# Performance work log

Hardware: AMD Instinct MI355X
Metric: run time of the kernel (lower is better)

## Reference

```python
import math
import jax, jax.numpy as jnp
import numpy as np

N_HEAD = 16
ROPE_BASE = 10000.0


def _rope_tables(T, half, dtype):
    # build_sin_cos(seq_len, dim=head_dim//2): inv freq of length `half`
    pos = jnp.arange(T, dtype=jnp.float32)[:, None]                       # (T,1)
    inv = jnp.exp(jnp.arange(0, 2 * half, 2, dtype=jnp.float32) * (-math.log(ROPE_BASE) / (2 * half)))
    ang = pos * inv                                                        # (T, half)
    return jnp.sin(ang).astype(dtype), jnp.cos(ang).astype(dtype)


def _apply_rope(q, k, sin, cos):
    # q,k: (B,T,H,Dh); sin,cos: (T, Dh//2) -> broadcast over batch and heads
    half = q.shape[-1] // 2
    s = sin[None, :, None, :]
    c = cos[None, :, None, :]
    q1, q2 = q[..., :half], q[..., half:]
    k1, k2 = k[..., :half], k[..., half:]
    q = jnp.concatenate([q1 * c - q2 * s, q2 * c + q1 * s], axis=-1)
    k = jnp.concatenate([k1 * c - k2 * s, k2 * c + k1 * s], axis=-1)
    return q, k


def setup_inputs() -> dict:
    key = jax.random.key(0)
    k1, k2, k3 = jax.random.split(key, 3)
    B, T, C = 2, 2048, 2048
    x = jax.random.normal(k1, (B, T, C), dtype=jnp.float32)
    w_qkv = jax.random.normal(k2, (3 * C, C), dtype=jnp.float32) * (1.0 / math.sqrt(C))
    w_proj = jax.random.normal(k3, (C, C), dtype=jnp.float32) * (1.0 / math.sqrt(C))
    return {"x": x, "w_qkv": w_qkv, "w_proj": w_proj}


def reference(x, w_qkv, w_proj):
    B, T, C = x.shape
    H = N_HEAD
    Dh = C // H
    # fused QKV projection (Linear, no bias): (B,T,3C) -> (B,T,3,H,Dh)
    qkv = jnp.einsum('btc,oc->bto', x, w_qkv).reshape(B, T, 3, H, Dh)
    q, k, v = qkv[:, :, 0], qkv[:, :, 1], qkv[:, :, 2]          # (B,T,H,Dh)
    sin, cos = _rope_tables(T, Dh // 2, x.dtype)
    q, k = _apply_rope(q, k, sin, cos)
    # causal attention, scale 1/sqrt(Dh) (flash default softmax_scale=None)
    scale = 1.0 / math.sqrt(Dh)
    scores = jnp.einsum('bqhd,bkhd->bhqk', q, k) * scale        # (B,H,T,T)
    mask = jnp.tril(jnp.ones((T, T), dtype=bool))
    scores = jnp.where(mask[None, None], scores, jnp.finfo(scores.dtype).min)
    probs = jax.nn.softmax(scores, axis=-1)
    out = jnp.einsum('bhqk,bkhd->bqhd', probs, v)               # (B,T,H,Dh)
    # faithful to original: permute(0,2,1,3) then reshape_as(x)
    out = jnp.transpose(out, (0, 2, 1, 3)).reshape(B, T, C)
    return jnp.einsum('btc,oc->bto', out, w_proj)
```

## Files before the change

kernel.cpp:

```cpp
#include <hip/hip_runtime.h>
#include <hip/hip_bf16.h>

typedef __bf16 bf16_t;
typedef __bf16 bf16x8 __attribute__((ext_vector_type(8)));
typedef float f32x4 __attribute__((ext_vector_type(4)));

#define MFMA16(a, b, c) __builtin_amdgcn_mfma_f32_16x16x32_bf16(a, b, c, 0, 0, 0)

__device__ __forceinline__ void async_copy16(const void* g, void* l) {
  __builtin_amdgcn_global_load_lds(
      (const __attribute__((address_space(1))) void*)g,
      (__attribute__((address_space(3))) void*)l, 16, 0, 0);
}

__global__ void cast_f32_bf16(const float* __restrict__ in, bf16_t* __restrict__ out, int n8) {
  int stride = gridDim.x * blockDim.x;
  for (int i = blockIdx.x * blockDim.x + threadIdx.x; i < n8; i += stride) {
    const float* p = in + (size_t)i * 8;
    f32x4 a = *(const f32x4*)p;
    f32x4 b = *(const f32x4*)(p + 4);
    bf16x8 o;
    o[0] = (bf16_t)a[0]; o[1] = (bf16_t)a[1]; o[2] = (bf16_t)a[2]; o[3] = (bf16_t)a[3];
    o[4] = (bf16_t)b[0]; o[5] = (bf16_t)b[1]; o[6] = (bf16_t)b[2]; o[7] = (bf16_t)b[3];
    *(bf16x8*)(out + (size_t)i * 8) = o;
  }
}

template <int MODE>
__global__ __launch_bounds__(512, 2) void gemm256(
    const bf16_t* __restrict__ A, const bf16_t* __restrict__ Bw, float* __restrict__ C,
    bf16_t* __restrict__ qo, bf16_t* __restrict__ ko, bf16_t* __restrict__ vto,
    int M, int N, int K, int nby) {
  __shared__ __align__(16) char lds[147456];
  int tid = threadIdx.x;
  int w = tid >> 6, lane = tid & 63;
  int wm = w >> 1, wn = w & 1;
  int mr = lane & 15, kg = lane >> 4;

  int nwg = gridDim.x;
  int orig = blockIdx.x;
  int wgid = (orig & 7) * (nwg >> 3) + (orig >> 3);
  int by = wgid % nby, bx = wgid / nby;
  int row0 = by * 256, col0 = bx * 128;

  size_t aoff[4], boff[2];
#pragma unroll
  for (int it = 0; it < 4; ++it) {
    int c = tid + it * 512;
    int r = c >> 3;
    int chs = (c & 7) ^ (r & 7);
    aoff[it] = (size_t)(row0 + r) * K + chs * 8;
  }
#pragma unroll
  for (int it = 0; it < 2; ++it) {
    int c = tid + it * 512;
    int r = c >> 3;
    int chs = (c & 7) ^ (r & 7);
    boff[it] = (size_t)(col0 + r) * K + chs * 8;
  }

  auto stageA = [&](int buf, int kt, int half) {
    char* Ad = &lds[buf * 49152];
#pragma unroll
    for (int it = half * 2; it < half * 2 + 2; ++it)
      async_copy16(A + aoff[it] + kt * 64, Ad + (tid + it * 512) * 16);
  };
  auto stageB = [&](int buf, int kt) {
    char* Bd = &lds[buf * 49152 + 32768];
#pragma unroll
    for (int it = 0; it < 2; ++it)
      async_copy16(Bw + boff[it] + kt * 64, Bd + (tid + it * 512) * 16);
  };

  f32x4 zero = {0.f, 0.f, 0.f, 0.f};
  f32x4 acc[4][4];
#pragma unroll
  for (int mi = 0; mi < 4; ++mi)
#pragma unroll
    for (int ni = 0; ni < 4; ++ni) acc[mi][ni] = zero;

  int nt = K >> 6;
  stageA(0, 0, 0); stageA(0, 0, 1); stageB(0, 0);
  stageA(1, 1, 0); stageA(1, 1, 1); stageB(1, 1);
  asm volatile("s_waitcnt vmcnt(6)" ::: "memory");
  __builtin_amdgcn_sched_barrier(0);
  __builtin_amdgcn_s_barrier();
  __builtin_amdgcn_sched_barrier(0);

#pragma unroll 1
  for (int t = 0; t < nt; ++t) {
    int cur = t % 3;
    int nxt = (t + 2) % 3;
    int kt2 = (t + 2 < nt) ? (t + 2) : t;
    const char* Ab = &lds[cur * 49152];
    const char* Bb = &lds[cur * 49152 + 32768];
    bf16x8 af[4][2], bfr[4][2];
#pragma unroll
    for (int mi = 0; mi < 4; ++mi) {
      int row = wm * 64 + mi * 16 + mr;
      const char* rb = Ab + row * 128;
      int sz = (row & 7) << 4;
      af[mi][0] = *(const bf16x8*)(rb + ((kg * 16) ^ sz));
      af[mi][1] = *(const bf16x8*)(rb + ((64 + kg * 16) ^ sz));
    }
#pragma unroll
    for (int ni = 0; ni < 4; ++ni) {
      int row = wn * 64 + ni * 16 + mr;
      const char* rb = Bb + row * 128;
      int sz = (row & 7) << 4;
      bfr[ni][0] = *(const bf16x8*)(rb + ((kg * 16) ^ sz));
      bfr[ni][1] = *(const bf16x8*)(rb + ((64 + kg * 16) ^ sz));
    }
    stageA(nxt, kt2, 0);
    __builtin_amdgcn_s_setprio(1);
#pragma unroll
    for (int mi = 0; mi < 4; ++mi) {
      acc[mi][0] = MFMA16(af[mi][0], bfr[0][0], acc[mi][0]);
      acc[mi][0] = MFMA16(af[mi][1], bfr[0][1], acc[mi][0]);
    }
    __builtin_amdgcn_s_setprio(0);
    stageA(nxt, kt2, 1);
    __builtin_amdgcn_s_setprio(1);
#pragma unroll
    for (int mi = 0; mi < 4; ++mi) {
      acc[mi][1] = MFMA16(af[mi][0], bfr[1][0], acc[mi][1]);
      acc[mi][1] = MFMA16(af[mi][1], bfr[1][1], acc[mi][1]);
    }
    __builtin_amdgcn_s_setprio(0);
    stageB(nxt, kt2);
    __builtin_amdgcn_s_setprio(1);
#pragma unroll
    for (int mi = 0; mi < 4; ++mi) {
      acc[mi][2] = MFMA16(af[mi][0], bfr[2][0], acc[mi][2]);
      acc[mi][2] = MFMA16(af[mi][1], bfr[2][1], acc[mi][2]);
      acc[mi][3] = MFMA16(af[mi][0], bfr[3][0], acc[mi][3]);
      acc[mi][3] = MFMA16(af[mi][1], bfr[3][1], acc[mi][3]);
    }
    __builtin_amdgcn_s_setprio(0);
    asm volatile("s_waitcnt vmcnt(6)" ::: "memory");
    __builtin_amdgcn_sched_barrier(0);
    __builtin_amdgcn_s_barrier();
    __builtin_amdgcn_sched_barrier(0);
  }
  asm volatile("s_waitcnt vmcnt(0)" ::: "memory");
  __syncthreads();

  if (MODE == 0) {
#pragma unroll
    for (int mi = 0; mi < 4; ++mi)
#pragma unroll
      for (int ni = 0; ni < 4; ++ni)
#pragma unroll
        for (int jj = 0; jj < 4; ++jj) {
          int row = row0 + wm * 64 + mi * 16 + kg * 4 + jj;
          int col = col0 + wn * 64 + ni * 16 + mr;
          C[(size_t)row * N + col] = acc[mi][ni][jj];
        }
  } else {
    char* tb = &lds[0];
    int s = col0 >> 11, h = (col0 >> 7) & 15;
    int b = row0 >> 11, t0 = row0 & 2047;
    if (s < 2) {
#pragma unroll
      for (int mi = 0; mi < 4; ++mi)
#pragma unroll
        for (int ni = 0; ni < 4; ++ni)
#pragma unroll
          for (int jj = 0; jj < 4; ++jj) {
            int rloc = wm * 64 + mi * 16 + kg * 4 + jj;
            int cb = (wn * 64 + ni * 16 + mr) * 2;
            *(bf16_t*)(tb + rloc * 256 + (cb ^ ((rloc & 7) << 4))) = (bf16_t)acc[mi][ni][jj];
          }
      __syncthreads();
      int r = tid >> 1, hh = tid & 1;
      const char* rowb = tb + r * 256;
      int sz = (r & 7) << 4;
      int t = t0 + r;
      bf16_t* dst = (s == 0 ? qo : ko) + ((size_t)((b * 16 + h) * 2048 + t)) * 128 + hh * 64;
      float tf = (float)t;
      const float cinv = -0.20762050593046014f;
#pragma unroll
      for (int m = 0; m < 8; ++m) {
        bf16x8 va = *(const bf16x8*)(rowb + ((hh * 128 + m * 16) ^ sz));
        bf16x8 vb = *(const bf16x8*)(rowb + (((hh ^ 1) * 128 + m * 16) ^ sz));
        bf16x8 o;
#pragma unroll
        for (int e = 0; e < 8; ++e) {
          float ang = tf * exp2f((float)(m * 8 + e) * cinv);
          float sv = __sinf(ang), cv = __cosf(ang);
          float x1 = (float)va[e], x2 = (float)vb[e];
          o[e] = (bf16_t)((hh == 0) ? (x1 * cv - x2 * sv) : (x1 * cv + x2 * sv));
        }
        *(bf16x8*)(dst + m * 8) = o;
      }
    } else {
#pragma unroll
      for (int mi = 0; mi < 4; ++mi)
#pragma unroll
        for (int ni = 0; ni < 4; ++ni)
#pragma unroll
          for (int jj = 0; jj < 4; ++jj) {
            int rloc = wm * 64 + mi * 16 + kg * 4 + jj;
            int cloc = wn * 64 + ni * 16 + mr;
            *(bf16_t*)(tb + cloc * 512 + ((rloc * 2) ^ ((cloc & 7) << 4))) =
                (bf16_t)acc[mi][ni][jj];
          }
      __syncthreads();
      int d = tid >> 2, qt = tid & 3;
      const char* rowb = tb + d * 512;
      int sz = (d & 7) << 4;
      bf16_t* dst = vto + ((size_t)((b * 16 + h) * 128 + d)) * 2048 + t0 + qt * 64;
#pragma unroll
      for (int m2 = 0; m2 < 8; ++m2)
        *(bf16x8*)(dst + m2 * 8) = *(const bf16x8*)(rowb + ((qt * 128 + m2 * 16) ^ sz));
    }
  }
}

__global__ __launch_bounds__(256) void attn_kernel(
    const bf16_t* __restrict__ qg, const bf16_t* __restrict__ kgl,
    const bf16_t* __restrict__ vtg, bf16_t* __restrict__ og) {
  __shared__ __align__(16) bf16_t Ks[2][64 * 128];
  __shared__ __align__(16) bf16_t Vs[2][128 * 64];
  __shared__ __align__(16) bf16_t plds[4][1024];
  const int T = 2048;
  int tid = threadIdx.x;
  int w = tid >> 6, lane = tid & 63;
  int mr = lane & 15, kg = lane >> 4;
  int swz = (mr & 7) << 4;

  int L = blockIdx.y * 16 + blockIdx.x;
  int role = (L & 7) * 64 + (L >> 3);
  int bx = role & 15, bh = role >> 4;

  const bf16_t* Q = qg + (size_t)bh * T * 128;
  const bf16_t* K = kgl + (size_t)bh * T * 128;
  const bf16_t* Vt = vtg + (size_t)bh * 128 * T;

  int sb = tid * 16;
  int krl = sb >> 8;
  int kc = (sb & 255) ^ ((krl & 7) << 4);
  size_t ksrc = (size_t)krl * 128 + (kc >> 1);
  int vdl = sb >> 7;
  int vc = (sb & 127) ^ ((vdl & 7) << 4);
  size_t vsrc = (size_t)vdl * 2048 + (vc >> 1);

  auto stage = [&](int buf, int kb) {
#pragma unroll
    for (int it = 0; it < 4; ++it)
      async_copy16(K + (size_t)(kb + it * 16) * 128 + ksrc, &Ks[buf][it * 2048 + tid * 8]);
#pragma unroll
    for (int it = 0; it < 4; ++it)
      async_copy16(Vt + (size_t)it * 65536 + kb + vsrc, &Vs[buf][it * 2048 + tid * 8]);
  };

  const float cscale = 0.12751744f;
  f32x4 zero = {0.f, 0.f, 0.f, 0.f};
  bf16_t* P = &plds[w][0];
  int b = bh >> 4, h = bh & 15;

#pragma unroll 1
  for (int ph = 0; ph < 2; ++ph) {
    int qb = ph ? bx : (31 - bx);
    int qr0 = qb * 64 + w * 16;
    bf16x8 qf[4];
#pragma unroll
    for (int db = 0; db < 4; ++db)
      qf[db] = *(const bf16x8*)(Q + (size_t)(qr0 + mr) * 128 + db * 32 + kg * 8);

    f32x4 acc[8];
#pragma unroll
    for (int d2 = 0; d2 < 8; ++d2) acc[d2] = zero;
    float mrun[4] = {-1e30f, -1e30f, -1e30f, -1e30f};
    float lrun[4] = {0.f, 0.f, 0.f, 0.f};

    int nj = qb + 1;
    __syncthreads();
    stage(0, 0);
    int cur = 0;
#pragma unroll 1
    for (int j = 0; j < nj; ++j) {
      __syncthreads();
      if (j + 1 < nj) stage(cur ^ 1, (j + 1) * 64);
      const char* KsB = (const char*)&Ks[cur][0];
      const char* VsB = (const char*)&Vs[cur][0];
      int kb = j * 64;
      f32x4 s[4];
#pragma unroll
      for (int ntl = 0; ntl < 4; ++ntl) {
        s[ntl] = zero;
        int rowb = (ntl * 16 + mr) * 256;
#pragma unroll
        for (int db = 0; db < 4; ++db) {
          bf16x8 kf = *(const bf16x8*)(KsB + rowb + ((db * 64 + kg * 16) ^ swz));
          s[ntl] = MFMA16(qf[db], kf, s[ntl]);
        }
      }
      float pvv[4][4];
      float tmax[4] = {-3e38f, -3e38f, -3e38f, -3e38f};
      bool diag = (j == qb);
#pragma unroll
      for (int ntl = 0; ntl < 4; ++ntl)
#pragma unroll
        for (int jj = 0; jj < 4; ++jj) {
          float v = s[ntl][jj] * cscale;
          if (diag && (kb + ntl * 16 + mr) > (qr0 + kg * 4 + jj)) v = -1e30f;
          pvv[ntl][jj] = v;
          tmax[jj] = fmaxf(tmax[jj], v);
        }
#pragma unroll
      for (int m = 1; m < 16; m <<= 1)
#pragma unroll
        for (int jj = 0; jj < 4; ++jj)
          tmax[jj] = fmaxf(tmax[jj], __shfl_xor(tmax[jj], m, 64));
      bool ok = true;
#pragma unroll
      for (int jj = 0; jj < 4; ++jj) ok &= (tmax[jj] <= mrun[jj] + 8.0f);
      if (!__all(ok)) {
#pragma unroll
        for (int jj = 0; jj < 4; ++jj) {
          float mn = fmaxf(mrun[jj], tmax[jj]);
          float corr = __builtin_amdgcn_exp2f(mrun[jj] - mn);
          mrun[jj] = mn;
          lrun[jj] *= corr;
#pragma unroll
          for (int d2 = 0; d2 < 8; ++d2) acc[d2][jj] *= corr;
        }
      }
      float rs[4] = {0.f, 0.f, 0.f, 0.f};
#pragma unroll
      for (int ntl = 0; ntl < 4; ++ntl)
#pragma unroll
        for (int jj = 0; jj < 4; ++jj) {
          float p = __builtin_amdgcn_exp2f(pvv[ntl][jj] - mrun[jj]);
          pvv[ntl][jj] = p;
          rs[jj] += p;
        }
#pragma unroll
      for (int m = 1; m < 16; m <<= 1)
#pragma unroll
        for (int jj = 0; jj < 4; ++jj) rs[jj] += __shfl_xor(rs[jj], m, 64);
#pragma unroll
      for (int jj = 0; jj < 4; ++jj) lrun[jj] += rs[jj];
#pragma unroll
      for (int ntl = 0; ntl < 4; ++ntl)
#pragma unroll
        for (int jj = 0; jj < 4; ++jj) {
          int rr = kg * 4 + jj;
          int cbyte = (mr + ntl * 16) * 2;
          *(bf16_t*)((char*)P + rr * 128 + (cbyte ^ ((rr & 7) << 4))) = (bf16_t)pvv[ntl][jj];
        }
#pragma unroll
      for (int ks = 0; ks < 2; ++ks) {
        int cb = (ks * 32 + kg * 8) * 2;
        bf16x8 pa = *(const bf16x8*)((const char*)P + mr * 128 + (cb ^ ((mr & 7) << 4)));
#pragma unroll
        for (int d2 = 0; d2 < 8; ++d2) {
          bf16x8 vf = *(const bf16x8*)(VsB + (d2 * 16 + mr) * 128 + ((ks * 64 + kg * 16) ^ swz));
          acc[d2] = MFMA16(pa, vf, acc[d2]);
        }
      }
      cur ^= 1;
    }
#pragma unroll
    for (int jj = 0; jj < 4; ++jj) {
      float invl = 1.0f / lrun[jj];
      int t = qr0 + kg * 4 + jj;
      size_t row = (size_t)b * 2048 + h * 128 + (t >> 4);
      bf16_t* orow = og + row * 2048 + (t & 15) * 128;
#pragma unroll
      for (int d2 = 0; d2 < 8; ++d2)
        orow[d2 * 16 + mr] = (bf16_t)(acc[d2][jj] * invl);
    }
  }
}

extern "C" void kernel_launch(void* const* d_in, const int* in_sizes, int n_in,
                              void* d_out, int out_size, void* d_ws, size_t ws_size,
                              hipStream_t stream) {
  const float* x = (const float*)d_in[0];
  const float* wqkv = (const float*)d_in[1];
  const float* wproj = (const float*)d_in[2];
  float* out = (float*)d_out;
  char* ws = (char*)d_ws;

  const size_t OFF_WQKV = 16777216;
  const size_t OFF_Q = 41943040;
  const size_t OFF_K = 58720256;
  const size_t OFF_VT = 75497472;

  bf16_t* xb = (bf16_t*)(ws);
  bf16_t* wqkvb = (bf16_t*)(ws + OFF_WQKV);
  bf16_t* g_q = (bf16_t*)(ws + OFF_Q);
  bf16_t* g_k = (bf16_t*)(ws + OFF_K);
  bf16_t* g_vt = (bf16_t*)(ws + OFF_VT);
  bf16_t* g_att = (bf16_t*)(ws);
  bf16_t* wprojb = (bf16_t*)(ws + OFF_WQKV);

  cast_f32_bf16<<<2048, 256, 0, stream>>>(x, xb, 8388608 / 8);
  cast_f32_bf16<<<2048, 256, 0, stream>>>(wqkv, wqkvb, 12582912 / 8);
  gemm256<1><<<768, 512, 0, stream>>>(xb, wqkvb, nullptr, g_q, g_k, g_vt,
                                      4096, 6144, 2048, 16);
  cast_f32_bf16<<<2048, 256, 0, stream>>>(wproj, wprojb, 4194304 / 8);
  attn_kernel<<<dim3(16, 32), 256, 0, stream>>>(g_q, g_k, g_vt, g_att);
  gemm256<0><<<256, 512, 0, stream>>>(g_att, wprojb, out, nullptr, nullptr, nullptr,
                                      4096, 2048, 2048, 16);
}
```

Before: 277.7 us.

## Add dedicated 256x256-tile QKV GEMM with 4-stage pipeline and fused RoPE epilogue

Replaces the templated 256x128-tile GEMM used for the QKV projection with a dedicated kernel that uses 256x256 output tiles, a 32-wide K step and a four-buffer async LDS pipeline, launched on 384 blocks instead of 768. Each block now covers two heads, so the RoPE epilogue writes both rotated halves per thread and the V-transpose epilogue covers two heads. The larger tile raises arithmetic intensity and halves the global reads per output. The cost is more accumulator registers per thread (128 floats) and fewer blocks to fill the CUs. The output-projection GEMM is trimmed to its plain fp32 store path.

```diff
diff --git a/kernel.cpp b/kernel.cpp
--- a/kernel.cpp
+++ b/kernel.cpp
@@ -26,10 +26,168 @@
   }
 }
 
+__global__ __launch_bounds__(512, 2) void gemm_qkv(
+    const bf16_t* __restrict__ A, const bf16_t* __restrict__ Bw,
+    bf16_t* __restrict__ qo, bf16_t* __restrict__ ko, bf16_t* __restrict__ vto,
+    int K) {
+  __shared__ __align__(16) char lds[131072];
+  int tid = threadIdx.x;
+  int w = tid >> 6, lane = tid & 63;
+  int wm = w & 1, wn = w >> 1;
+  int mr = lane & 15, kg = lane >> 4;
+
+  int orig = blockIdx.x;
+  int chunk = orig & 7, i = orig >> 3;
+  int by = (chunk & 3) * 4 + (i & 3);
+  int bx = (chunk >> 2) * 12 + (i >> 2);
+  int row0 = by * 256, col0 = bx * 256;
+
+  size_t aoff[2], boff[2];
+#pragma unroll
+  for (int it = 0; it < 2; ++it) {
+    int c = tid + it * 512;
+    int r = c >> 2;
+    int lc = (c & 3) ^ ((r >> 1) & 3);
+    aoff[it] = (size_t)(row0 + r) * K + lc * 8;
+    boff[it] = (size_t)(col0 + r) * K + lc * 8;
+  }
+
+  auto stageA = [&](int buf, int kt) {
+    char* Ad = &lds[buf * 32768];
+#pragma unroll
+    for (int it = 0; it < 2; ++it)
+      async_copy16(A + aoff[it] + kt * 32, Ad + (tid + it * 512) * 16);
+  };
+  auto stageB = [&](int buf, int kt) {
+    char* Bd = &lds[buf * 32768 + 16384];
+#pragma unroll
+    for (int it = 0; it < 2; ++it)
+      async_copy16(Bw + boff[it] + kt * 32, Bd + (tid + it * 512) * 16);
+  };
+
+  f32x4 zero = {0.f, 0.f, 0.f, 0.f};
+  f32x4 acc[8][4];
+#pragma unroll
+  for (int mi = 0; mi < 8; ++mi)
+#pragma unroll
+    for (int ni = 0; ni < 4; ++ni) acc[mi][ni] = zero;
+
+  int nt = K >> 5;
+  stageA(0, 0); stageB(0, 0);
+  stageA(1, 1); stageB(1, 1);
+  stageA(2, 2); stageB(2, 2);
+  asm volatile("s_waitcnt vmcnt(8)" ::: "memory");
+  __builtin_amdgcn_sched_barrier(0);
+  __builtin_amdgcn_s_barrier();
+  __builtin_amdgcn_sched_barrier(0);
+
+#pragma unroll 1
+  for (int t = 0; t < nt; ++t) {
+    int cur = t & 3;
+    int nb = (t + 3) & 3;
+    int kt3 = (t + 3 < nt) ? (t + 3) : (nt - 1);
+    const char* Ab = &lds[cur * 32768];
+    const char* Bb = &lds[cur * 32768 + 16384];
+    bf16x8 af[8], bfr[4];
+#pragma unroll
+    for (int mi = 0; mi < 8; ++mi) {
+      int r = wm * 128 + mi * 16 + mr;
+      af[mi] = *(const bf16x8*)(Ab + r * 64 + ((kg ^ ((r >> 1) & 3)) << 4));
+    }
+#pragma unroll
+    for (int ni = 0; ni < 4; ++ni) {
+      int r = wn * 64 + ni * 16 + mr;
+      bfr[ni] = *(const bf16x8*)(Bb + r * 64 + ((kg ^ ((r >> 1) & 3)) << 4));
+    }
+    stageA(nb, kt3);
+    __builtin_amdgcn_s_setprio(1);
+#pragma unroll
+    for (int mi = 0; mi < 8; ++mi) acc[mi][0] = MFMA16(af[mi], bfr[0], acc[mi][0]);
+#pragma unroll
+    for (int mi = 0; mi < 8; ++mi) acc[mi][1] = MFMA16(af[mi], bfr[1], acc[mi][1]);
+    __builtin_amdgcn_s_setprio(0);
+    stageB(nb, kt3);
+    __builtin_amdgcn_s_setprio(1);
+#pragma unroll
+    for (int mi = 0; mi < 8; ++mi) acc[mi][2] = MFMA16(af[mi], bfr[2], acc[mi][2]);
+#pragma unroll
+    for (int mi = 0; mi < 8; ++mi) acc[mi][3] = MFMA16(af[mi], bfr[3], acc[mi][3]);
+    __builtin_amdgcn_s_setprio(0);
+    asm volatile("s_waitcnt vmcnt(8)" ::: "memory");
+    __builtin_amdgcn_sched_barrier(0);
+    __builtin_amdgcn_s_barrier();
+    __builtin_amdgcn_sched_barrier(0);
+  }
+  asm volatile("s_waitcnt vmcnt(0)" ::: "memory");
+  __syncthreads();
+
+  char* tb = &lds[0];
+  int s = col0 >> 11;
+  int h0 = (col0 >> 7) & 15;
+  int b = row0 >> 11, t0 = row0 & 2047;
+  if (s < 2) {
+#pragma unroll
+    for (int mi = 0; mi < 8; ++mi)
+#pragma unroll
+      for (int ni = 0; ni < 4; ++ni)
+#pragma unroll
+        for (int jj = 0; jj < 4; ++jj) {
+          int rl = wm * 128 + mi * 16 + kg * 4 + jj;
+          int cb = (wn * 64 + ni * 16 + mr) * 2;
+          *(bf16_t*)(tb + rl * 512 + (cb ^ ((rl & 7) << 4))) = (bf16_t)acc[mi][ni][jj];
+        }
+    __syncthreads();
+    int r = tid >> 1, hs = tid & 1;
+    const char* rowb = tb + r * 512;
+    int sz = (r & 7) << 4;
+    int t = t0 + r;
+    bf16_t* dst = (s == 0 ? qo : ko) + ((size_t)((b * 16 + h0 + hs) * 2048 + t)) * 128;
+    float tf = (float)t;
+    const float cinv = -0.20762050593046014f;
+    bf16x8 vin[16];
+#pragma unroll
+    for (int m = 0; m < 16; ++m)
+      vin[m] = *(const bf16x8*)(rowb + ((hs * 256 + m * 16) ^ sz));
+#pragma unroll
+    for (int m = 0; m < 8; ++m) {
+      bf16x8 o1, o2;
+#pragma unroll
+      for (int e = 0; e < 8; ++e) {
+        float ang = tf * exp2f((float)(m * 8 + e) * cinv);
+        float sv = __sinf(ang), cv = __cosf(ang);
+        float x1 = (float)vin[m][e], x2 = (float)vin[m + 8][e];
+        o1[e] = (bf16_t)(x1 * cv - x2 * sv);
+        o2[e] = (bf16_t)(x2 * cv + x1 * sv);
+      }
+      *(bf16x8*)(dst + m * 8) = o1;
+      *(bf16x8*)(dst + 64 + m * 8) = o2;
+    }
+  } else {
+#pragma unroll
+    for (int mi = 0; mi < 8; ++mi)
+#pragma unroll
+      for (int ni = 0; ni < 4; ++ni)
+#pragma unroll
+        for (int jj = 0; jj < 4; ++jj) {
+          int rl = wm * 128 + mi * 16 + kg * 4 + jj;
+          int cl = wn * 64 + ni * 16 + mr;
+          *(bf16_t*)(tb + cl * 512 + ((rl * 2) ^ ((cl & 7) << 4))) = (bf16_t)acc[mi][ni][jj];
+        }
+    __syncthreads();
+    int d = tid >> 1, ts = tid & 1;
+    const char* rowb = tb + d * 512;
+    int sz = (d & 7) << 4;
+    bf16_t* dst = vto + ((size_t)((b * 16 + h0 + (d >> 7)) * 128 + (d & 127))) * 2048 +
+                  t0 + ts * 128;
+#pragma unroll
+    for (int m = 0; m < 16; ++m)
+      *(bf16x8*)(dst + m * 8) = *(const bf16x8*)(rowb + ((ts * 256 + m * 16) ^ sz));
+  }
+}
+
 template <int MODE>
 __global__ __launch_bounds__(512, 2) void gemm256(
     const bf16_t* __restrict__ A, const bf16_t* __restrict__ Bw, float* __restrict__ C,
-    bf16_t* __restrict__ qo, bf16_t* __restrict__ ko, bf16_t* __restrict__ vto,
     int M, int N, int K, int nby) {
   __shared__ __align__(16) char lds[147456];
   int tid = threadIdx.x;
@@ -145,76 +303,16 @@
   asm volatile("s_waitcnt vmcnt(0)" ::: "memory");
   __syncthreads();
 
-  if (MODE == 0) {
-#pragma unroll
-    for (int mi = 0; mi < 4; ++mi)
-#pragma unroll
-      for (int ni = 0; ni < 4; ++ni)
-#pragma unroll
-        for (int jj = 0; jj < 4; ++jj) {
-          int row = row0 + wm * 64 + mi * 16 + kg * 4 + jj;
-          int col = col0 + wn * 64 + ni * 16 + mr;
-          C[(size_t)row * N + col] = acc[mi][ni][jj];
-        }
-  } else {
-    char* tb = &lds[0];
-    int s = col0 >> 11, h = (col0 >> 7) & 15;
-    int b = row0 >> 11, t0 = row0 & 2047;
-    if (s < 2) {
-#pragma unroll
-      for (int mi = 0; mi < 4; ++mi)
-#pragma unroll
-        for (int ni = 0; ni < 4; ++ni)
-#pragma unroll
-          for (int jj = 0; jj < 4; ++jj) {
-            int rloc = wm * 64 + mi * 16 + kg * 4 + jj;
-            int cb = (wn * 64 + ni * 16 + mr) * 2;
-            *(bf16_t*)(tb + rloc * 256 + (cb ^ ((rloc & 7) << 4))) = (bf16_t)acc[mi][ni][jj];
-          }
-      __syncthreads();
-      int r = tid >> 1, hh = tid & 1;
-      const char* rowb = tb + r * 256;
-      int sz = (r & 7) << 4;
-      int t = t0 + r;
-      bf16_t* dst = (s == 0 ? qo : ko) + ((size_t)((b * 16 + h) * 2048 + t)) * 128 + hh * 64;
-      float tf = (float)t;
-      const float cinv = -0.20762050593046014f;
-#pragma unroll
-      for (int m = 0; m < 8; ++m) {
-        bf16x8 va = *(const bf16x8*)(rowb + ((hh * 128 + m * 16) ^ sz));
-        bf16x8 vb = *(const bf16x8*)(rowb + (((hh ^ 1) * 128 + m * 16) ^ sz));
-        bf16x8 o;
-#pragma unroll
-        for (int e = 0; e < 8; ++e) {
-          float ang = tf * exp2f((float)(m * 8 + e) * cinv);
-          float sv = __sinf(ang), cv = __cosf(ang);
-          float x1 = (float)va[e], x2 = (float)vb[e];
-          o[e] = (bf16_t)((hh == 0) ? (x1 * cv - x2 * sv) : (x1 * cv + x2 * sv));
-        }
-        *(bf16x8*)(dst + m * 8) = o;
+#pragma unroll
+  for (int mi = 0; mi < 4; ++mi)
+#pragma unroll
+    for (int ni = 0; ni < 4; ++ni)
+#pragma unroll
+      for (int jj = 0; jj < 4; ++jj) {
+        int row = row0 + wm * 64 + mi * 16 + kg * 4 + jj;
+        int col = col0 + wn * 64 + ni * 16 + mr;
+        C[(size_t)row * N + col] = acc[mi][ni][jj];
       }
-    } else {
-#pragma unroll
-      for (int mi = 0; mi < 4; ++mi)
-#pragma unroll
-        for (int ni = 0; ni < 4; ++ni)
-#pragma unroll
-          for (int jj = 0; jj < 4; ++jj) {
-            int rloc = wm * 64 + mi * 16 + kg * 4 + jj;
-            int cloc = wn * 64 + ni * 16 + mr;
-            *(bf16_t*)(tb + cloc * 512 + ((rloc * 2) ^ ((cloc & 7) << 4))) =
-                (bf16_t)acc[mi][ni][jj];
-          }
-      __syncthreads();
-      int d = tid >> 2, qt = tid & 3;
-      const char* rowb = tb + d * 512;
-      int sz = (d & 7) << 4;
-      bf16_t* dst = vto + ((size_t)((b * 16 + h) * 128 + d)) * 2048 + t0 + qt * 64;
-#pragma unroll
-      for (int m2 = 0; m2 < 8; ++m2)
-        *(bf16x8*)(dst + m2 * 8) = *(const bf16x8*)(rowb + ((qt * 128 + m2 * 16) ^ sz));
-    }
-  }
 }
 
 __global__ __launch_bounds__(256) void attn_kernel(
@@ -399,10 +497,8 @@
 
   cast_f32_bf16<<<2048, 256, 0, stream>>>(x, xb, 8388608 / 8);
   cast_f32_bf16<<<2048, 256, 0, stream>>>(wqkv, wqkvb, 12582912 / 8);
-  gemm256<1><<<768, 512, 0, stream>>>(xb, wqkvb, nullptr, g_q, g_k, g_vt,
-                                      4096, 6144, 2048, 16);
+  gemm_qkv<<<384, 512, 0, stream>>>(xb, wqkvb, g_q, g_k, g_vt, 2048);
   cast_f32_bf16<<<2048, 256, 0, stream>>>(wproj, wprojb, 4194304 / 8);
   attn_kernel<<<dim3(16, 32), 256, 0, stream>>>(g_q, g_k, g_vt, g_att);
-  gemm256<0><<<256, 512, 0, stream>>>(g_att, wprojb, out, nullptr, nullptr, nullptr,
-                                      4096, 2048, 2048, 16);
+  gemm256<0><<<256, 512, 0, stream>>>(g_att, wprojb, out, 4096, 2048, 2048, 16);
 }
```

Measured after the change: 277.5 us. No clear change (-0.1%).
